# Performance work log

Hardware: AMD Instinct MI355X
Metric: run time of the kernel (lower is better)

## Reference

```python
import jax, jax.numpy as jnp
import numpy as np

D_MODEL = 1024
NUM_HEADS = 16
D_K = D_MODEL // NUM_HEADS


def setup_inputs() -> dict:
    key = jax.random.key(0)
    ks = jax.random.split(key, 8)
    B, S, D = 4, 2048, D_MODEL
    scale = 1.0 / np.sqrt(D)
    return {
        "query": jax.random.normal(ks[0], (B, S, D), dtype=jnp.float32),
        "key": jax.random.normal(ks[1], (B, S, D), dtype=jnp.float32),
        "value": jax.random.normal(ks[2], (B, S, D), dtype=jnp.float32),
        "Wq": jax.random.normal(ks[3], (D, D), dtype=jnp.float32) * scale,
        "bq": jnp.zeros((D,), dtype=jnp.float32),
        "Wk": jax.random.normal(ks[4], (D, D), dtype=jnp.float32) * scale,
        "bk": jnp.zeros((D,), dtype=jnp.float32),
        "Wv": jax.random.normal(ks[5], (D, D), dtype=jnp.float32) * scale,
        "bv": jnp.zeros((D,), dtype=jnp.float32),
        "Wo": jax.random.normal(ks[6], (D, D), dtype=jnp.float32) * scale,
        "bo": jnp.zeros((D,), dtype=jnp.float32),
    }


def reference(query, key, value, Wq, bq, Wk, bk, Wv, bv, Wo, bo):
    B, S, D = query.shape
    H, dk = NUM_HEADS, D_K

    def proj(x, W, b):
        # nn.Linear: x @ W.T + b, then split heads -> [B, H, S, dk]
        y = jnp.einsum("bsd,ed->bse", x, W) + b
        return y.reshape(B, -1, H, dk).transpose(0, 2, 1, 3)

    Q = proj(query, Wq, bq)
    K = proj(key, Wk, bk)
    V = proj(value, Wv, bv)

    scores = jnp.einsum("bhqd,bhkd->bhqk", Q, K) / np.sqrt(dk).astype(jnp.float32)
    attn = jax.nn.softmax(scores, axis=-1)
    out = jnp.einsum("bhqk,bhkd->bhqd", attn, V)  # [B, H, S, dk]
    out = out.transpose(0, 2, 1, 3).reshape(B, -1, D)
    return jnp.einsum("bsd,ed->bse", out, Wo) + bo
```

## Files before the change

### kernel.cpp

```cpp
#include <hip/hip_runtime.h>
#include <hip/hip_bf16.h>

typedef unsigned short u16;
typedef __attribute__((ext_vector_type(8))) short bf16x8;
typedef __attribute__((ext_vector_type(4))) short bf16x4;
typedef __attribute__((ext_vector_type(4))) float f32x4;

#define LOG2E_OVER8 0.18033688011112043f

__device__ __forceinline__ float ex2(float x) {
#if __has_builtin(__builtin_amdgcn_exp2f)
    return __builtin_amdgcn_exp2f(x);
#else
    float r;
    asm volatile("v_exp_f32 %0, %1" : "=v"(r) : "v"(x));
    return r;
#endif
}

__device__ __forceinline__ u16 f2bf(float f) {
    unsigned u = __float_as_uint(f);
    u += 0x7FFFu + ((u >> 16) & 1u);
    return (u16)(u >> 16);
}

__device__ __forceinline__ unsigned pk_rtz(float lo, float hi) {
    return __builtin_amdgcn_perm(__float_as_uint(hi), __float_as_uint(lo), 0x07060302u);
}
__device__ __forceinline__ bf16x8 pack8(float a0, float a1, float a2, float a3,
                                        float a4, float a5, float a6, float a7) {
    unsigned p[4];
    p[0] = pk_rtz(a0, a1);
    p[1] = pk_rtz(a2, a3);
    p[2] = pk_rtz(a4, a5);
    p[3] = pk_rtz(a6, a7);
    bf16x8 r;
    __builtin_memcpy(&r, p, 16);
    return r;
}

__device__ __forceinline__ f32x4 mfma32(bf16x8 a, bf16x8 b, f32x4 c) {
    return __builtin_amdgcn_mfma_f32_16x16x32_bf16(a, b, c, 0, 0, 0);
}

__device__ __forceinline__ void gload16(const void* g, void* l) {
    __builtin_amdgcn_global_load_lds((const __attribute__((address_space(1))) unsigned int*)g,
                                     (__attribute__((address_space(3))) unsigned int*)l,
                                     16, 0, 0);
}

__global__ __launch_bounds__(256) void cvt_x3(const float* __restrict__ a, const float* __restrict__ b,
                                              const float* __restrict__ c, u16* __restrict__ out) {
    const float* src = (blockIdx.y == 0) ? a : (blockIdx.y == 1) ? b : c;
    size_t i = ((size_t)blockIdx.x * 256 + threadIdx.x) * 4;
    float4 v = *(const float4*)(src + i);
    bf16x4 o;
    o[0] = (short)f2bf(v.x); o[1] = (short)f2bf(v.y);
    o[2] = (short)f2bf(v.z); o[3] = (short)f2bf(v.w);
    *(bf16x4*)(out + (size_t)blockIdx.y * (8192ull * 1024) + i) = o;
}
__global__ __launch_bounds__(256) void cvt_w4(const float* __restrict__ a, const float* __restrict__ b,
                                              const float* __restrict__ c, const float* __restrict__ d,
                                              u16* __restrict__ out) {
    const float* src = (blockIdx.y == 0) ? a : (blockIdx.y == 1) ? b : (blockIdx.y == 2) ? c : d;
    size_t i = ((size_t)blockIdx.x * 256 + threadIdx.x) * 4;
    float4 v = *(const float4*)(src + i);
    bf16x4 o;
    o[0] = (short)f2bf(v.x); o[1] = (short)f2bf(v.y);
    o[2] = (short)f2bf(v.z); o[3] = (short)f2bf(v.w);
    *(bf16x4*)(out + (size_t)blockIdx.y * (1024ull * 1024) + i) = o;
}

struct GemmAcc { f32x4 a[4][4]; };

__device__ __forceinline__ void gemm_core(const u16* __restrict__ A, const u16* __restrict__ Bt,
                                          u16* As, u16* Bs, int bm, int bn, GemmAcc& acc) {
    constexpr int K = 1024;
    const int tid = threadIdx.x;
    const int lane = tid & 63;
    const int lr = lane & 15, lg = lane >> 4;

    for (int i = 0; i < 4; i++)
        for (int j = 0; j < 4; j++) acc.a[i][j] = (f32x4){0.f, 0.f, 0.f, 0.f};

    const int row0 = tid >> 2, u0 = tid & 3;
    const int su = (u0 ^ ((row0 >> 1) & 3)) * 8;
    const size_t a_off0 = (size_t)(bm + row0) * K + su;
    const size_t a_off1 = (size_t)(bm + 64 + row0) * K + su;
    const size_t b_off0 = (size_t)(bn + row0) * K + su;
    const size_t b_off1 = (size_t)(bn + 64 + row0) * K + su;
    const int c0 = tid * 8, c1 = (256 + tid) * 8;

    const int fu = (lg ^ ((lr >> 1) & 3)) * 8;
    const int wid = tid >> 6, wr = wid >> 1, wc = wid & 1;

    for (int kt = 0; kt < K; kt += 32) {
        gload16(A + a_off0 + kt, &As[c0]);
        gload16(A + a_off1 + kt, &As[c1]);
        gload16(Bt + b_off0 + kt, &Bs[c0]);
        gload16(Bt + b_off1 + kt, &Bs[c1]);
        __syncthreads();
        bf16x8 aF[4], bF[4];
#pragma unroll
        for (int mi = 0; mi < 4; mi++) aF[mi] = *(const bf16x8*)&As[(wr * 64 + mi * 16 + lr) * 32 + fu];
#pragma unroll
        for (int ni = 0; ni < 4; ni++) bF[ni] = *(const bf16x8*)&Bs[(wc * 64 + ni * 16 + lr) * 32 + fu];
#pragma unroll
        for (int mi = 0; mi < 4; mi++)
#pragma unroll
            for (int ni = 0; ni < 4; ni++) acc.a[mi][ni] = mfma32(aF[mi], bF[ni], acc.a[mi][ni]);
        __syncthreads();
    }
}

template<int MODE>
__global__ __launch_bounds__(256) void gemm_bt(const u16* __restrict__ A, const u16* __restrict__ Bt,
                                               const float* __restrict__ bias, void* __restrict__ Cout,
                                               float scale) {
    __shared__ u16 As[128 * 32];
    __shared__ u16 Bs[128 * 32];
    const int bm = blockIdx.y * 128, bn = blockIdx.x * 128;
    GemmAcc acc;
    gemm_core(A, Bt, As, Bs, bm, bn, acc);

    const int lane = threadIdx.x & 63, wid = threadIdx.x >> 6;
    const int wr = wid >> 1, wc = wid & 1;
    const int lr = lane & 15, lg = lane >> 4;

#pragma unroll
    for (int ni = 0; ni < 4; ni++) {
        const int n = bn + wc * 64 + ni * 16 + lr;
        const float bv = bias[n];
#pragma unroll
        for (int mi = 0; mi < 4; mi++) {
            const int mbase = bm + wr * 64 + mi * 16 + lg * 4;
#pragma unroll
            for (int r = 0; r < 4; r++) {
                const int m = mbase + r;
                const float v = acc.a[mi][ni][r] + bv;
                if (MODE == 0) {
                    ((float*)Cout)[(size_t)m * 1024 + n] = v;
                } else if (MODE == 1) {
                    ((u16*)Cout)[(size_t)m * 1024 + n] = f2bf(v * scale);
                } else {
                    const int bq_ = m >> 11, kk = m & 2047, kb = kk >> 6, k64 = kk & 63;
                    const int hh = n >> 6, dd = n & 63;
                    const int ks = k64 >> 4, g = (k64 >> 2) & 3, rr = k64 & 3;
                    const int unit = ((ks >> 1) << 2) | g;
                    const int jj = ((ks & 1) << 2) | rr;
                    ((u16*)Cout)[((size_t)((bq_ * 16 + hh) * 32 + kb)) * 4096 +
                                 dd * 64 + ((unit ^ (dd & 7)) << 3) + jj] = f2bf(v);
                }
            }
        }
    }
}

__global__ __launch_bounds__(256) void attn_fwd(const u16* __restrict__ Qp, const u16* __restrict__ Kp,
                                                const u16* __restrict__ VTb, u16* __restrict__ AO) {
    __shared__ u16 kt[2][4096];
    __shared__ u16 vt[2][4096];
    const int tid = threadIdx.x;
    const int lane = tid & 63, wave = tid >> 6;
    const int lr = lane & 15, lg = lane >> 4;
    const int l7 = lr & 7;
    const int bh = blockIdx.x & 63, b = bh >> 4, h = bh & 15;
    const int q0 = (blockIdx.x >> 6) * 128 + wave * 32;

    const u16* qbase = Qp + (size_t)(b * 2048 + q0) * 1024 + h * 64;
    bf16x8 qf[2][2];
#pragma unroll
    for (int qt = 0; qt < 2; qt++)
#pragma unroll
        for (int hf = 0; hf < 2; hf++)
            qf[qt][hf] = *(const bf16x8*)(qbase + (size_t)(qt * 16 + lr) * 1024 + hf * 32 + lg * 8);

    const int srow = tid >> 3;
    const int scol = (((tid & 7) ^ (srow & 7)) * 8);
    const u16* kg = Kp + (size_t)(b * 2048 + srow) * 1024 + h * 64 + scol;
    const u16* vg = VTb + (size_t)(b * 16 + h) * 32 * 4096 + tid * 8;
    const int ldst = tid * 8;

#define STAGE(buf, kb_)                                                       \
    do {                                                                      \
        gload16(kg + (size_t)(kb_) * 64 * 1024,        &kt[buf][ldst]);       \
        gload16(kg + (size_t)((kb_) * 64 + 32) * 1024, &kt[buf][2048 + ldst]);\
        gload16(vg + (size_t)(kb_) * 4096,             &vt[buf][ldst]);       \
        gload16(vg + (size_t)(kb_) * 4096 + 2048,      &vt[buf][2048 + ldst]);\
    } while (0)

    f32x4 lsacc[2];
    f32x4 ot[2][4];
#pragma unroll
    for (int qt = 0; qt < 2; qt++) {
        lsacc[qt] = (f32x4){0.f, 0.f, 0.f, 0.f};
#pragma unroll
        for (int dt = 0; dt < 4; dt++) ot[qt][dt] = (f32x4){0.f, 0.f, 0.f, 0.f};
    }

    bf16x8 ones8;
#pragma unroll
    for (int i = 0; i < 8; i++) ones8[i] = (short)0x3F80;

    STAGE(0, 0);
    __syncthreads();
    int cur = 0;

    const f32x4 zero = (f32x4){0.f, 0.f, 0.f, 0.f};
    const int ku0 = (lg ^ l7) * 8;
    const int ku1 = ((4 + lg) ^ l7) * 8;

#pragma unroll 2
    for (int it = 0; it < 32; ++it) {
        if (it < 31) STAGE(cur ^ 1, it + 1);

        const u16* kl = &kt[cur][0];
        const u16* vl = &vt[cur][0];

        f32x4 s[2][4];
        __builtin_amdgcn_s_setprio(1);
#pragma unroll
        for (int ks = 0; ks < 4; ++ks) {
            const int rbase = (ks * 16 + lr) * 64;
            bf16x8 kf0 = *(const bf16x8*)&kl[rbase + ku0];
            bf16x8 kf1 = *(const bf16x8*)&kl[rbase + ku1];
            s[0][ks] = mfma32(kf0, qf[0][0], zero);
            s[0][ks] = mfma32(kf1, qf[0][1], s[0][ks]);
            s[1][ks] = mfma32(kf0, qf[1][0], zero);
            s[1][ks] = mfma32(kf1, qf[1][1], s[1][ks]);
        }
        __builtin_amdgcn_s_setprio(0);

        bf16x8 pf[2][2];
#pragma unroll
        for (int qt = 0; qt < 2; ++qt) {
            const f32x4* sq = s[qt];
#pragma unroll
            for (int kh = 0; kh < 2; ++kh) {
                const f32x4 sa = sq[2 * kh], sb = sq[2 * kh + 1];
                pf[qt][kh] = pack8(ex2(sa[0]), ex2(sa[1]), ex2(sa[2]), ex2(sa[3]),
                                   ex2(sb[0]), ex2(sb[1]), ex2(sb[2]), ex2(sb[3]));
                lsacc[qt] = mfma32(ones8, pf[qt][kh], lsacc[qt]);
            }
        }

        __builtin_amdgcn_s_setprio(1);
#pragma unroll
        for (int dt = 0; dt < 4; ++dt) {
            const int vrow = (dt * 16 + lr) * 64;
            bf16x8 vf0 = *(const bf16x8*)&vl[vrow + ku0];
            bf16x8 vf1 = *(const bf16x8*)&vl[vrow + ku1];
            ot[0][dt] = mfma32(vf0, pf[0][0], ot[0][dt]);
            ot[0][dt] = mfma32(vf1, pf[0][1], ot[0][dt]);
            ot[1][dt] = mfma32(vf0, pf[1][0], ot[1][dt]);
            ot[1][dt] = mfma32(vf1, pf[1][1], ot[1][dt]);
        }
        __builtin_amdgcn_s_setprio(0);

        __syncthreads();
        cur ^= 1;
    }

    const float inv0 = 1.0f / lsacc[0][0], inv1 = 1.0f / lsacc[1][0];
    u16* t_ = &kt[0][0] + wave * 2048;
#pragma unroll
    for (int qt = 0; qt < 2; ++qt) {
        const float inv = qt ? inv1 : inv0;
#pragma unroll
        for (int dt = 0; dt < 4; ++dt)
#pragma unroll
            for (int r = 0; r < 4; ++r)
                t_[(qt * 16 + lr) * 64 + dt * 16 + lg * 4 + r] = f2bf(ot[qt][dt][r] * inv);
    }
    __syncthreads();
    const int qq = lane >> 1, dseg = (lane & 1) * 32;
    u16* dst = AO + (size_t)(b * 2048 + q0 + qq) * 1024 + h * 64 + dseg;
    bf16x8 o_[4];
#pragma unroll
    for (int j = 0; j < 4; ++j) o_[j] = *(const bf16x8*)&t_[qq * 64 + dseg + j * 8];
#pragma unroll
    for (int j = 0; j < 4; ++j) *(bf16x8*)(dst + j * 8) = o_[j];
#undef STAGE
}

extern "C" void kernel_launch(void* const* d_in, const int* in_sizes, int n_in,
                              void* d_out, int out_size, void* d_ws, size_t ws_size,
                              hipStream_t stream) {
    const float* q_in = (const float*)d_in[0];
    const float* k_in = (const float*)d_in[1];
    const float* v_in = (const float*)d_in[2];
    const float* Wq = (const float*)d_in[3];
    const float* bq = (const float*)d_in[4];
    const float* Wk = (const float*)d_in[5];
    const float* bk = (const float*)d_in[6];
    const float* Wv = (const float*)d_in[7];
    const float* bv = (const float*)d_in[8];
    const float* Wo = (const float*)d_in[9];
    const float* bo = (const float*)d_in[10];

    const size_t MD = (size_t)8192 * 1024;
    const size_t DD = (size_t)1024 * 1024;
    u16* ws = (u16*)d_ws;
    u16* Xq = ws;
    u16* Xk = Xq + MD;
    u16* Xv = Xk + MD;
    u16* Wqb = Xq + 3 * MD;
    u16* Wkb = Wqb + DD;
    u16* Wvb = Wkb + DD;
    u16* Wob = Wvb + DD;
    u16* Qp = Wqb + 4 * DD;
    u16* Kp = Qp + MD;
    u16* VTb = Kp + MD;
    u16* AO = VTb + MD;

    cvt_x3<<<dim3(8192, 3), 256, 0, stream>>>(q_in, k_in, v_in, Xq);
    cvt_w4<<<dim3(1024, 4), 256, 0, stream>>>(Wq, Wk, Wv, Wo, Wqb);

    dim3 gg(8, 64);
    gemm_bt<1><<<gg, 256, 0, stream>>>(Xq, Wqb, bq, Qp, LOG2E_OVER8);
    gemm_bt<1><<<gg, 256, 0, stream>>>(Xk, Wkb, bk, Kp, 1.0f);
    gemm_bt<2><<<gg, 256, 0, stream>>>(Xv, Wvb, bv, VTb, 1.0f);

    attn_fwd<<<1024, 256, 0, stream>>>(Qp, Kp, VTb, AO);

    gemm_bt<0><<<gg, 256, 0, stream>>>(AO, Wob, bo, (float*)d_out, 1.0f);
}
```

Baseline: 221.9 us.

## Double query rows per attention wave and merge conversion kernels

Each attention wave now handles 64 query rows instead of 32, so each block covers 256 queries and the grid halves to 512 blocks. Every K/V tile staged in LDS is reused across twice as many queries, which halves K/V global traffic and staging syncs. The cost is higher register pressure (more accumulators and score tiles) and fewer blocks on a large-CU GPU. The two fp32-to-bf16 conversion kernels are also merged into one launch to save launch overhead.

New measurement: 205.5 us. 7.4% less time.

```diff
diff --git a/kernel.cpp b/kernel.cpp
--- a/kernel.cpp
+++ b/kernel.cpp
@@ -49,26 +49,31 @@
                                      16, 0, 0);
 }
 
-__global__ __launch_bounds__(256) void cvt_x3(const float* __restrict__ a, const float* __restrict__ b,
-                                              const float* __restrict__ c, u16* __restrict__ out) {
-    const float* src = (blockIdx.y == 0) ? a : (blockIdx.y == 1) ? b : c;
-    size_t i = ((size_t)blockIdx.x * 256 + threadIdx.x) * 4;
-    float4 v = *(const float4*)(src + i);
+__global__ __launch_bounds__(256) void cvt_all(const float* __restrict__ q, const float* __restrict__ k,
+                                               const float* __restrict__ v, const float* __restrict__ wq,
+                                               const float* __restrict__ wk, const float* __restrict__ wv,
+                                               const float* __restrict__ wo, u16* __restrict__ xout,
+                                               u16* __restrict__ wout) {
+    const int bid = blockIdx.x;
+    const float* src;
+    u16* dst;
+    size_t off;
+    if (bid < 24576) {
+        const int t = bid >> 13, c = bid & 8191;
+        src = (t == 0) ? q : (t == 1) ? k : v;
+        dst = xout + (size_t)t * (8192ull * 1024);
+        off = (size_t)c * 1024 + threadIdx.x * 4;
+    } else {
+        const int t = (bid - 24576) >> 10, c = (bid - 24576) & 1023;
+        src = (t == 0) ? wq : (t == 1) ? wk : (t == 2) ? wv : wo;
+        dst = wout + (size_t)t * (1024ull * 1024);
+        off = (size_t)c * 1024 + threadIdx.x * 4;
+    }
+    float4 val = *(const float4*)(src + off);
     bf16x4 o;
-    o[0] = (short)f2bf(v.x); o[1] = (short)f2bf(v.y);
-    o[2] = (short)f2bf(v.z); o[3] = (short)f2bf(v.w);
-    *(bf16x4*)(out + (size_t)blockIdx.y * (8192ull * 1024) + i) = o;
-}
-__global__ __launch_bounds__(256) void cvt_w4(const float* __restrict__ a, const float* __restrict__ b,
-                                              const float* __restrict__ c, const float* __restrict__ d,
-                                              u16* __restrict__ out) {
-    const float* src = (blockIdx.y == 0) ? a : (blockIdx.y == 1) ? b : (blockIdx.y == 2) ? c : d;
-    size_t i = ((size_t)blockIdx.x * 256 + threadIdx.x) * 4;
-    float4 v = *(const float4*)(src + i);
-    bf16x4 o;
-    o[0] = (short)f2bf(v.x); o[1] = (short)f2bf(v.y);
-    o[2] = (short)f2bf(v.z); o[3] = (short)f2bf(v.w);
-    *(bf16x4*)(out + (size_t)blockIdx.y * (1024ull * 1024) + i) = o;
+    o[0] = (short)f2bf(val.x); o[1] = (short)f2bf(val.y);
+    o[2] = (short)f2bf(val.z); o[3] = (short)f2bf(val.w);
+    *(bf16x4*)(dst + off) = o;
 }
 
 struct GemmAcc { f32x4 a[4][4]; };
@@ -156,8 +161,8 @@
     }
 }
 
-__global__ __launch_bounds__(256) void attn_fwd(const u16* __restrict__ Qp, const u16* __restrict__ Kp,
-                                                const u16* __restrict__ VTb, u16* __restrict__ AO) {
+__global__ __launch_bounds__(256, 2) void attn_fwd(const u16* __restrict__ Qp, const u16* __restrict__ Kp,
+                                                   const u16* __restrict__ VTb, u16* __restrict__ AO) {
     __shared__ u16 kt[2][4096];
     __shared__ u16 vt[2][4096];
     const int tid = threadIdx.x;
@@ -165,12 +170,12 @@
     const int lr = lane & 15, lg = lane >> 4;
     const int l7 = lr & 7;
     const int bh = blockIdx.x & 63, b = bh >> 4, h = bh & 15;
-    const int q0 = (blockIdx.x >> 6) * 128 + wave * 32;
+    const int q0 = (blockIdx.x >> 6) * 256 + wave * 64;
 
     const u16* qbase = Qp + (size_t)(b * 2048 + q0) * 1024 + h * 64;
-    bf16x8 qf[2][2];
-#pragma unroll
-    for (int qt = 0; qt < 2; qt++)
+    bf16x8 qf[4][2];
+#pragma unroll
+    for (int qt = 0; qt < 4; qt++)
 #pragma unroll
         for (int hf = 0; hf < 2; hf++)
             qf[qt][hf] = *(const bf16x8*)(qbase + (size_t)(qt * 16 + lr) * 1024 + hf * 32 + lg * 8);
@@ -189,10 +194,10 @@
         gload16(vg + (size_t)(kb_) * 4096 + 2048,      &vt[buf][2048 + ldst]);\
     } while (0)
 
-    f32x4 lsacc[2];
-    f32x4 ot[2][4];
-#pragma unroll
-    for (int qt = 0; qt < 2; qt++) {
+    f32x4 lsacc[4];
+    f32x4 ot[4][4];
+#pragma unroll
+    for (int qt = 0; qt < 4; qt++) {
         lsacc[qt] = (f32x4){0.f, 0.f, 0.f, 0.f};
 #pragma unroll
         for (int dt = 0; dt < 4; dt++) ot[qt][dt] = (f32x4){0.f, 0.f, 0.f, 0.f};
@@ -217,27 +222,27 @@
         const u16* kl = &kt[cur][0];
         const u16* vl = &vt[cur][0];
 
-        f32x4 s[2][4];
+        f32x4 s[4][4];
         __builtin_amdgcn_s_setprio(1);
 #pragma unroll
         for (int ks = 0; ks < 4; ++ks) {
             const int rbase = (ks * 16 + lr) * 64;
             bf16x8 kf0 = *(const bf16x8*)&kl[rbase + ku0];
             bf16x8 kf1 = *(const bf16x8*)&kl[rbase + ku1];
-            s[0][ks] = mfma32(kf0, qf[0][0], zero);
-            s[0][ks] = mfma32(kf1, qf[0][1], s[0][ks]);
-            s[1][ks] = mfma32(kf0, qf[1][0], zero);
-            s[1][ks] = mfma32(kf1, qf[1][1], s[1][ks]);
+#pragma unroll
+            for (int qt = 0; qt < 4; ++qt) {
+                s[qt][ks] = mfma32(kf0, qf[qt][0], zero);
+                s[qt][ks] = mfma32(kf1, qf[qt][1], s[qt][ks]);
+            }
         }
         __builtin_amdgcn_s_setprio(0);
 
-        bf16x8 pf[2][2];
-#pragma unroll
-        for (int qt = 0; qt < 2; ++qt) {
-            const f32x4* sq = s[qt];
+        bf16x8 pf[4][2];
+#pragma unroll
+        for (int qt = 0; qt < 4; ++qt) {
 #pragma unroll
             for (int kh = 0; kh < 2; ++kh) {
-                const f32x4 sa = sq[2 * kh], sb = sq[2 * kh + 1];
+                const f32x4 sa = s[qt][2 * kh], sb = s[qt][2 * kh + 1];
                 pf[qt][kh] = pack8(ex2(sa[0]), ex2(sa[1]), ex2(sa[2]), ex2(sa[3]),
                                    ex2(sb[0]), ex2(sb[1]), ex2(sb[2]), ex2(sb[3]));
                 lsacc[qt] = mfma32(ones8, pf[qt][kh], lsacc[qt]);
@@ -250,10 +255,11 @@
             const int vrow = (dt * 16 + lr) * 64;
             bf16x8 vf0 = *(const bf16x8*)&vl[vrow + ku0];
             bf16x8 vf1 = *(const bf16x8*)&vl[vrow + ku1];
-            ot[0][dt] = mfma32(vf0, pf[0][0], ot[0][dt]);
-            ot[0][dt] = mfma32(vf1, pf[0][1], ot[0][dt]);
-            ot[1][dt] = mfma32(vf0, pf[1][0], ot[1][dt]);
-            ot[1][dt] = mfma32(vf1, pf[1][1], ot[1][dt]);
+#pragma unroll
+            for (int qt = 0; qt < 4; ++qt) {
+                ot[qt][dt] = mfma32(vf0, pf[qt][0], ot[qt][dt]);
+                ot[qt][dt] = mfma32(vf1, pf[qt][1], ot[qt][dt]);
+            }
         }
         __builtin_amdgcn_s_setprio(0);
 
@@ -261,25 +267,31 @@
         cur ^= 1;
     }
 
-    const float inv0 = 1.0f / lsacc[0][0], inv1 = 1.0f / lsacc[1][0];
+    float inv[4];
+#pragma unroll
+    for (int qt = 0; qt < 4; qt++) inv[qt] = 1.0f / lsacc[qt][0];
     u16* t_ = &kt[0][0] + wave * 2048;
 #pragma unroll
-    for (int qt = 0; qt < 2; ++qt) {
-        const float inv = qt ? inv1 : inv0;
-#pragma unroll
-        for (int dt = 0; dt < 4; ++dt)
-#pragma unroll
-            for (int r = 0; r < 4; ++r)
-                t_[(qt * 16 + lr) * 64 + dt * 16 + lg * 4 + r] = f2bf(ot[qt][dt][r] * inv);
-    }
-    __syncthreads();
-    const int qq = lane >> 1, dseg = (lane & 1) * 32;
-    u16* dst = AO + (size_t)(b * 2048 + q0 + qq) * 1024 + h * 64 + dseg;
-    bf16x8 o_[4];
-#pragma unroll
-    for (int j = 0; j < 4; ++j) o_[j] = *(const bf16x8*)&t_[qq * 64 + dseg + j * 8];
-#pragma unroll
-    for (int j = 0; j < 4; ++j) *(bf16x8*)(dst + j * 8) = o_[j];
+    for (int pass = 0; pass < 2; ++pass) {
+        __syncthreads();
+#pragma unroll
+        for (int qh = 0; qh < 2; ++qh) {
+            const int qt = pass * 2 + qh;
+#pragma unroll
+            for (int dt = 0; dt < 4; ++dt)
+#pragma unroll
+                for (int r = 0; r < 4; ++r)
+                    t_[(qh * 16 + lr) * 64 + dt * 16 + lg * 4 + r] = f2bf(ot[qt][dt][r] * inv[qt]);
+        }
+        __syncthreads();
+        const int qq = lane >> 1, dseg = (lane & 1) * 32;
+        u16* dst = AO + (size_t)(b * 2048 + q0 + pass * 32 + qq) * 1024 + h * 64 + dseg;
+        bf16x8 o_[4];
+#pragma unroll
+        for (int j = 0; j < 4; ++j) o_[j] = *(const bf16x8*)&t_[qq * 64 + dseg + j * 8];
+#pragma unroll
+        for (int j = 0; j < 4; ++j) *(bf16x8*)(dst + j * 8) = o_[j];
+    }
 #undef STAGE
 }
 
@@ -313,15 +325,14 @@
     u16* VTb = Kp + MD;
     u16* AO = VTb + MD;
 
-    cvt_x3<<<dim3(8192, 3), 256, 0, stream>>>(q_in, k_in, v_in, Xq);
-    cvt_w4<<<dim3(1024, 4), 256, 0, stream>>>(Wq, Wk, Wv, Wo, Wqb);
+    cvt_all<<<28672, 256, 0, stream>>>(q_in, k_in, v_in, Wq, Wk, Wv, Wo, Xq, Wqb);
 
     dim3 gg(8, 64);
     gemm_bt<1><<<gg, 256, 0, stream>>>(Xq, Wqb, bq, Qp, LOG2E_OVER8);
     gemm_bt<1><<<gg, 256, 0, stream>>>(Xk, Wkb, bk, Kp, 1.0f);
     gemm_bt<2><<<gg, 256, 0, stream>>>(Xv, Wvb, bv, VTb, 1.0f);
 
-    attn_fwd<<<1024, 256, 0, stream>>>(Qp, Kp, VTb, AO);
+    attn_fwd<<<512, 256, 0, stream>>>(Qp, Kp, VTb, AO);
 
     gemm_bt<0><<<gg, 256, 0, stream>>>(AO, Wob, bo, (float*)d_out, 1.0f);
 }
```
